# Kernel tuning notes

Measured on AMD Instinct MI355X. Metric: run time of the kernel, lower is better.

## Reference

```python
import jax, jax.numpy as jnp
import numpy as np

NUM_ITERATIONS = 10


def _nearest_neighbor(src, tgt):
    # src: [B,N,3], tgt: [B,M,3] -> indices [B,N] of nearest tgt point per src point
    inner = -2.0 * jnp.einsum('bnd,bmd->bnm', src, tgt)            # [B,N,M]
    xx = jnp.sum(src * src, axis=2, keepdims=True)                  # [B,N,1]
    yy = jnp.sum(tgt * tgt, axis=2, keepdims=True).transpose(0, 2, 1)  # [B,1,M]
    distances = xx + inner + yy                                     # [B,N,M]
    return jnp.argmin(distances, axis=2)                            # [B,N]


def _compute_transformation(src, tgt):
    # src, tgt: [B,N,3] matched pairs -> rigid (R [B,3,3], t [B,3])
    N = src.shape[1]
    c_src = jnp.mean(src, axis=1, keepdims=True)                    # [B,1,3]
    c_tgt = jnp.mean(tgt, axis=1, keepdims=True)                    # [B,1,3]
    H = jnp.einsum('bnd,bne->bde', src - c_src, tgt - c_tgt) / N    # [B,3,3]
    U, S, Vh = jnp.linalg.svd(H, full_matrices=False)
    V = jnp.swapaxes(Vh, -1, -2)                                    # matches torch.svd's V
    R = V @ jnp.swapaxes(U, -1, -2)
    det = jnp.linalg.det(R)                                         # [B]
    sign = 1.0 - 2.0 * (det < 0).astype(src.dtype)                  # +1 or -1
    # torch code scales V[:, :, 2] (third column of V)
    V = V * jnp.concatenate([jnp.ones_like(sign)[:, None],
                             jnp.ones_like(sign)[:, None],
                             sign[:, None]], axis=1)[:, None, :]    # scale col 2
    R = V @ jnp.swapaxes(U, -1, -2)                                 # [B,3,3]
    t = c_tgt[:, 0, :] - jnp.einsum('bij,bj->bi', R, c_src[:, 0, :])  # [B,3]
    return R, t


def _icp(src, tgt):
    transformed_src = src
    R = None
    t = None
    for _ in range(NUM_ITERATIONS):
        indices = _nearest_neighbor(transformed_src, tgt)           # [B,N]
        matched_tgt = jnp.take_along_axis(tgt, indices[:, :, None], axis=1)  # [B,N,3]
        R, t = _compute_transformation(transformed_src, matched_tgt)
        # faithful to torch: x @ R + t (R applied on the right)
        transformed_src = jnp.einsum('bnd,bde->bne', transformed_src, R) + t[:, None, :]
    return R, t, transformed_src


def setup_inputs() -> dict:
    key = jax.random.key(0)
    k1, k2 = jax.random.split(key)
    src = jax.random.normal(k1, (4, 4096, 3), dtype=jnp.float32)
    tgt = jax.random.normal(k2, (4, 4096, 3), dtype=jnp.float32)
    return {"src": src, "tgt": tgt}


def reference(src, tgt):
    # Returns (est_R [B,3,3], est_t [B,3], transformed_source [B,N,3])
    return _icp(src, tgt)
```

## Files before the change

kernel.cpp:

```cpp
#include <hip/hip_runtime.h>
#include <math.h>

#define NB 4
#define NP 4096
#define MP 4096

typedef __bf16 bf16x8 __attribute__((ext_vector_type(8)));
typedef float  f32x16 __attribute__((ext_vector_type(16)));

static __device__ __forceinline__ unsigned short bh(float f) {
    unsigned u = __float_as_uint(f);
    unsigned r = (u + 0x7FFFu + ((u >> 16) & 1u)) >> 16;
    return (unsigned short)r;
}
static __device__ __forceinline__ float hf(unsigned short h) {
    return __uint_as_float(((unsigned)h) << 16);
}

__device__ __forceinline__ void kabsch_f32(const float* s, float* RtL) {
    const float invN = 1.0f / (float)NP;
    float cs[3] = { s[0] * invN, s[1] * invN, s[2] * invN };
    float ct[3] = { s[3] * invN, s[4] * invN, s[5] * invN };
    float H[3][3];
    for (int d = 0; d < 3; ++d)
        for (int e = 0; e < 3; ++e)
            H[d][e] = s[6 + d * 3 + e] * invN - cs[d] * ct[e];

    float A[3][3];
    for (int i = 0; i < 3; ++i)
        for (int j = 0; j < 3; ++j)
            A[i][j] = H[0][i] * H[0][j] + H[1][i] * H[1][j] + H[2][i] * H[2][j];

    float V[3][3] = {{1, 0, 0}, {0, 1, 0}, {0, 0, 1}};
    for (int sweep = 0; sweep < 8; ++sweep) {
        float off = A[0][1] * A[0][1] + A[0][2] * A[0][2] + A[1][2] * A[1][2];
        if (off < 1e-16f) break;
        for (int pi = 0; pi < 3; ++pi) {
            const int p = (pi == 2) ? 1 : 0;
            const int q = (pi == 0) ? 1 : 2;
            float apq = A[p][q];
            if (fabsf(apq) < 1e-30f) continue;
            float theta = (A[q][q] - A[p][p]) / (2.0f * apq);
            float t = 1.0f / (fabsf(theta) + sqrtf(1.0f + theta * theta));
            if (theta < 0.0f) t = -t;
            float cth = 1.0f / sqrtf(1.0f + t * t);
            float sth = t * cth;
            float App = A[p][p], Aqq = A[q][q];
            A[p][p] = App - t * apq;
            A[q][q] = Aqq + t * apq;
            A[p][q] = A[q][p] = 0.0f;
            const int r = 3 - p - q;
            float Apr = A[p][r], Aqr = A[q][r];
            A[p][r] = A[r][p] = cth * Apr - sth * Aqr;
            A[q][r] = A[r][q] = sth * Apr + cth * Aqr;
            for (int i = 0; i < 3; ++i) {
                float Vip = V[i][p], Viq = V[i][q];
                V[i][p] = cth * Vip - sth * Viq;
                V[i][q] = sth * Vip + cth * Viq;
            }
        }
    }
    float lam[3] = { A[0][0], A[1][1], A[2][2] };
    for (int i = 0; i < 2; ++i)
        for (int j = i + 1; j < 3; ++j)
            if (lam[j] > lam[i]) {
                float tl = lam[i]; lam[i] = lam[j]; lam[j] = tl;
                for (int k = 0; k < 3; ++k) {
                    float tv = V[k][i]; V[k][i] = V[k][j]; V[k][j] = tv;
                }
            }

    float U[3][3];
    for (int k = 0; k < 3; ++k) {
        float w0 = H[0][0] * V[0][k] + H[0][1] * V[1][k] + H[0][2] * V[2][k];
        float w1 = H[1][0] * V[0][k] + H[1][1] * V[1][k] + H[1][2] * V[2][k];
        float w2 = H[2][0] * V[0][k] + H[2][1] * V[1][k] + H[2][2] * V[2][k];
        float nrm = sqrtf(w0 * w0 + w1 * w1 + w2 * w2);
        if (nrm > 1e-20f) {
            U[0][k] = w0 / nrm; U[1][k] = w1 / nrm; U[2][k] = w2 / nrm;
        } else {
            U[0][k] = U[1][0] * U[2][1] - U[2][0] * U[1][1];
            U[1][k] = U[2][0] * U[0][1] - U[0][0] * U[2][1];
            U[2][k] = U[0][0] * U[1][1] - U[1][0] * U[0][1];
        }
    }

    float detH = H[0][0] * (H[1][1] * H[2][2] - H[1][2] * H[2][1])
               - H[0][1] * (H[1][0] * H[2][2] - H[1][2] * H[2][0])
               + H[0][2] * (H[1][0] * H[2][1] - H[1][1] * H[2][0]);
    float sgn = (detH < 0.0f) ? -1.0f : 1.0f;

    float R[3][3];
    for (int i = 0; i < 3; ++i)
        for (int j = 0; j < 3; ++j)
            R[i][j] = V[i][0] * U[j][0] + V[i][1] * U[j][1] + sgn * V[i][2] * U[j][2];
    float tv[3];
    for (int i = 0; i < 3; ++i)
        tv[i] = ct[i] - (R[i][0] * cs[0] + R[i][1] * cs[1] + R[i][2] * cs[2]);

    for (int i = 0; i < 3; ++i)
        for (int j = 0; j < 3; ++j)
            RtL[i * 3 + j] = R[i][j];
    for (int i = 0; i < 3; ++i) RtL[9 + i] = tv[i];
}

__global__ __launch_bounds__(256) void icp_init(const float* __restrict__ tgt,
                                                float4* __restrict__ tgt4,
                                                uint4* __restrict__ Bbuf) {
    const int t    = blockIdx.x * 256 + threadIdx.x;
    const int b    = t >> 13;
    const int rem  = t & 8191;
    const int tile = rem >> 6;
    const int lane = rem & 63;
    const int n    = lane & 31;
    const int h    = lane >> 5;
    const int gt   = b * MP + tile * 32 + n;

    float x = tgt[gt * 3 + 0];
    float y = tgt[gt * 3 + 1];
    float z = tgt[gt * 3 + 2];
    float wv = x * x + y * y + z * z;

    unsigned short xh = bh(x), xl = bh(x - hf(xh));
    unsigned short yh = bh(y), yl = bh(y - hf(yh));
    unsigned short zh = bh(z), zl = bh(z - hf(zh));
    unsigned short wh = bh(wv), wl = bh(wv - hf(wh));
    const unsigned short ONE = 0x3F80;

    unsigned short s0, s1, s2, s3, s4, s5, s6, s7;
    if (h == 0) { s0 = xh; s1 = xh; s2 = xl; s3 = xl;
                  s4 = yh; s5 = yh; s6 = yl; s7 = yl; }
    else        { s0 = zh; s1 = zh; s2 = zl; s3 = zl;
                  s4 = wh; s5 = wl; s6 = ONE; s7 = ONE; }
    uint4 u;
    u.x = (unsigned)s0 | ((unsigned)s1 << 16);
    u.y = (unsigned)s2 | ((unsigned)s3 << 16);
    u.z = (unsigned)s4 | ((unsigned)s5 << 16);
    u.w = (unsigned)s6 | ((unsigned)s7 << 16);
    Bbuf[t] = u;

    if (h == 0) tgt4[gt] = make_float4(x, y, z, wv);
}

__global__ __launch_bounds__(1024) void icp_scan(
        const float* __restrict__ src,
        const float4* __restrict__ tgt4,
        const uint4* __restrict__ Bbuf,
        float* __restrict__ S,
        const float* __restrict__ pprev,
        float* __restrict__ pout,
        int first) {
    __shared__ unsigned CK[512];
    __shared__ float RtL[12];

    const int blk = blockIdx.x;
    const int b   = blk >> 6;
    const int g   = blk & 63;
    const int tid = threadIdx.x;
    const int w   = tid >> 6;
    const int l   = tid & 63;
    const int ts  = w & 1;
    const int tr  = w >> 1;
    const int gsrc = b * NP + g * 64 + l;

    if (w == 0) {
        if (first) {
            if (l < 12) RtL[l] = (l == 0 || l == 4 || l == 8) ? 1.0f : 0.0f;
        } else {
            const float4* rp = (const float4*)(pprev + (b * 64 + l) * 16);
            float4 r0 = rp[0], r1 = rp[1], r2 = rp[2], r3 = rp[3];
            float sm[15] = { r0.x, r0.y, r0.z, r0.w, r1.x, r1.y, r1.z, r1.w,
                             r2.x, r2.y, r2.z, r2.w, r3.x, r3.y, r3.z };
            #pragma unroll
            for (int k = 0; k < 15; ++k) {
                float v = sm[k];
                v += __shfl_down(v, 32);
                v += __shfl_down(v, 16);
                v += __shfl_down(v, 8);
                v += __shfl_down(v, 4);
                v += __shfl_down(v, 2);
                v += __shfl_down(v, 1);
                sm[k] = v;
            }
            if (l == 0) kabsch_f32(sm, RtL);
        }
    }
    __syncthreads();

    float px, py, pz;
    {
        const float* P = first ? src : S;
        float x = P[gsrc * 3 + 0];
        float y = P[gsrc * 3 + 1];
        float z = P[gsrc * 3 + 2];
        px = x * RtL[0] + y * RtL[3] + z * RtL[6] + RtL[9];
        py = x * RtL[1] + y * RtL[4] + z * RtL[7] + RtL[10];
        pz = x * RtL[2] + y * RtL[5] + z * RtL[8] + RtL[11];
    }
    if (w == 1) {
        S[gsrc * 3 + 0] = px;
        S[gsrc * 3 + 1] = py;
        S[gsrc * 3 + 2] = pz;
    }

    const int h = l >> 5;
    union { unsigned short s[8]; bf16x8 v; } Af;
    {
        const int j3 = ts * 32 + (l & 31);
        float pxj = __shfl(px, j3);
        float pyj = __shfl(py, j3);
        float pzj = __shfl(pz, j3);
        float ax = -2.0f * pxj, ay = -2.0f * pyj, az = -2.0f * pzj;
        float qv = pxj * pxj + pyj * pyj + pzj * pzj + 1.0f;
        unsigned short axh = bh(ax), axl = bh(ax - hf(axh));
        unsigned short ayh = bh(ay), ayl = bh(ay - hf(ayh));
        unsigned short azh = bh(az), azl = bh(az - hf(azh));
        unsigned short qh  = bh(qv), ql  = bh(qv - hf(qh));
        const unsigned short ONE = 0x3F80;
        if (h == 0) {
            Af.s[0] = axh; Af.s[1] = axl; Af.s[2] = axh; Af.s[3] = axl;
            Af.s[4] = ayh; Af.s[5] = ayl; Af.s[6] = ayh; Af.s[7] = ayl;
        } else {
            Af.s[0] = azh; Af.s[1] = azl; Af.s[2] = azh; Af.s[3] = azl;
            Af.s[4] = ONE; Af.s[5] = ONE; Af.s[6] = qh;  Af.s[7] = ql;
        }
    }

    f32x16 zero;
    #pragma unroll
    for (int i = 0; i < 16; ++i) zero[i] = 0.0f;

    float best[16];
    #pragma unroll
    for (int r = 0; r < 16; ++r) best[r] = __uint_as_float(0x7F7FFFFFu);

    const uint4* Bw = Bbuf + (b * 128 + tr * 16) * 64;
    const int col = l & 31;

    uint4 fb[4];
    fb[0] = Bw[l];
    fb[1] = Bw[64 + l];
    fb[2] = Bw[128 + l];
    fb[3] = Bw[192 + l];

    #pragma unroll
    for (int t = 0; t < 16; ++t) {
        bf16x8 Bf = __builtin_bit_cast(bf16x8, fb[t & 3]);
        if (t < 12) fb[t & 3] = Bw[(t + 4) * 64 + l];
        f32x16 d16 = __builtin_amdgcn_mfma_f32_32x32x16_bf16(Af.v, Bf, zero,
                                                             0, 0, 0);
        const unsigned idxk = (unsigned)((tr * 16 + t) * 32 + col);
        #pragma unroll
        for (int r = 0; r < 16; ++r) {
            float key = __uint_as_float(
                (__float_as_uint(d16[r]) & 0xFFFFF000u) | idxk);
            best[r] = fminf(best[r], key);
        }
    }

    #pragma unroll
    for (int r = 0; r < 16; ++r) {
        float v = best[r];
        v = fminf(v, __shfl_xor(v, 1));
        v = fminf(v, __shfl_xor(v, 2));
        v = fminf(v, __shfl_xor(v, 4));
        v = fminf(v, __shfl_xor(v, 8));
        v = fminf(v, __shfl_xor(v, 16));
        best[r] = v;
    }
    if ((l & 31) == 0) {
        #pragma unroll
        for (int r = 0; r < 16; ++r) {
            const int row = (r & 3) + 8 * (r >> 2) + 4 * h;
            CK[tr * 64 + ts * 32 + row] = __float_as_uint(best[r]);
        }
    }
    __syncthreads();

    if (w == 0) {
        unsigned kb = CK[l];
        #pragma unroll
        for (int k = 1; k < 8; ++k) {
            unsigned kk = CK[k * 64 + l];
            kb = kk < kb ? kk : kb;
        }
        const int idx = kb & 0xFFF;
        float4 mt = tgt4[b * MP + idx];
        const float tx = mt.x, ty = mt.y, tz = mt.z;

        float v[15];
        v[0]  = px;      v[1]  = py;      v[2]  = pz;
        v[3]  = tx;      v[4]  = ty;      v[5]  = tz;
        v[6]  = px * tx; v[7]  = px * ty; v[8]  = px * tz;
        v[9]  = py * tx; v[10] = py * ty; v[11] = py * tz;
        v[12] = pz * tx; v[13] = pz * ty; v[14] = pz * tz;
        #pragma unroll
        for (int k = 0; k < 15; ++k) {
            float s = v[k];
            s += __shfl_down(s, 32);
            s += __shfl_down(s, 16);
            s += __shfl_down(s, 8);
            s += __shfl_down(s, 4);
            s += __shfl_down(s, 2);
            s += __shfl_down(s, 1);
            v[k] = s;
        }
        if (l == 0) {
            float* pp = pout + blk * 16;
            #pragma unroll
            for (int k = 0; k < 15; ++k) pp[k] = v[k];
        }
    }
}

__global__ __launch_bounds__(256) void icp_final(
        const float* __restrict__ S,
        const float* __restrict__ plast,
        float* __restrict__ out) {
    __shared__ float RtL[12];
    const int bk  = blockIdx.x;
    const int tid = threadIdx.x;
    const int gid = bk * 256 + tid;
    const int b   = gid >> 12;

    if (tid < 64) {
        const float4* rp = (const float4*)(plast + (b * 64 + tid) * 16);
        float4 r0 = rp[0], r1 = rp[1], r2 = rp[2], r3 = rp[3];
        float sm[15] = { r0.x, r0.y, r0.z, r0.w, r1.x, r1.y, r1.z, r1.w,
                         r2.x, r2.y, r2.z, r2.w, r3.x, r3.y, r3.z };
        #pragma unroll
        for (int k = 0; k < 15; ++k) {
            float v = sm[k];
            v += __shfl_down(v, 32);
            v += __shfl_down(v, 16);
            v += __shfl_down(v, 8);
            v += __shfl_down(v, 4);
            v += __shfl_down(v, 2);
            v += __shfl_down(v, 1);
            sm[k] = v;
        }
        if (tid == 0) kabsch_f32(sm, RtL);
    }
    __syncthreads();

    float x = S[gid * 3 + 0];
    float y = S[gid * 3 + 1];
    float z = S[gid * 3 + 2];
    out[48 + gid * 3 + 0] = x * RtL[0] + y * RtL[3] + z * RtL[6] + RtL[9];
    out[48 + gid * 3 + 1] = x * RtL[1] + y * RtL[4] + z * RtL[7] + RtL[10];
    out[48 + gid * 3 + 2] = x * RtL[2] + y * RtL[5] + z * RtL[8] + RtL[11];
    if ((bk & 15) == 0) {
        if (tid < 9) out[b * 9 + tid] = RtL[tid];
        if (tid < 3) out[36 + b * 3 + tid] = RtL[9 + tid];
    }
}

extern "C" void kernel_launch(void* const* d_in, const int* in_sizes, int n_in,
                              void* d_out, int out_size, void* d_ws, size_t ws_size,
                              hipStream_t stream) {
    const float* src = (const float*)d_in[0];
    const float* tgt = (const float*)d_in[1];
    float* out = (float*)d_out;

    float* W     = (float*)d_ws;
    float4* tgt4 = (float4*)W;
    uint4*  Bbuf = (uint4*)(W + 65536);
    float*  S    = W + 65536 + 131072;
    float*  pA   = S + 49152;
    float*  pB   = pA + 4096;
    float* bufs[2] = { pA, pB };

    icp_init<<<128, 256, 0, stream>>>(tgt, tgt4, Bbuf);
    for (int k = 0; k < 10; ++k) {
        icp_scan<<<256, 1024, 0, stream>>>(src, tgt4, Bbuf, S,
                                           bufs[(k + 1) & 1], bufs[k & 1],
                                           k == 0 ? 1 : 0);
    }
    icp_final<<<64, 256, 0, stream>>>(S, bufs[1], out);
}
```

Baseline: 193.7 us.

## Fuse per-iteration Kabsch into last-block reduction and track cumulative transform

```diff
diff --git a/kernel.cpp b/kernel.cpp
--- a/kernel.cpp
+++ b/kernel.cpp
@@ -32,7 +32,7 @@
             A[i][j] = H[0][i] * H[0][j] + H[1][i] * H[1][j] + H[2][i] * H[2][j];
 
     float V[3][3] = {{1, 0, 0}, {0, 1, 0}, {0, 0, 1}};
-    for (int sweep = 0; sweep < 8; ++sweep) {
+    for (int sweep = 0; sweep < 6; ++sweep) {
         float off = A[0][1] * A[0][1] + A[0][2] * A[0][2] + A[1][2] * A[1][2];
         if (off < 1e-16f) break;
         for (int pi = 0; pi < 3; ++pi) {
@@ -106,7 +106,10 @@
 
 __global__ __launch_bounds__(256) void icp_init(const float* __restrict__ tgt,
                                                 float4* __restrict__ tgt4,
-                                                uint4* __restrict__ Bbuf) {
+                                                uint4* __restrict__ Bbuf,
+                                                float* __restrict__ acc,
+                                                unsigned* __restrict__ cnt,
+                                                float* __restrict__ Rc) {
     const int t    = blockIdx.x * 256 + threadIdx.x;
     const int b    = t >> 13;
     const int rem  = t & 8191;
@@ -138,80 +141,62 @@
     u.z = (unsigned)s4 | ((unsigned)s5 << 16);
     u.w = (unsigned)s6 | ((unsigned)s7 << 16);
     Bbuf[t] = u;
-
     if (h == 0) tgt4[gt] = make_float4(x, y, z, wv);
-}
-
-__global__ __launch_bounds__(1024) void icp_scan(
+
+    if (blockIdx.x == 0) {
+        const int td = threadIdx.x;
+        for (int k = td; k < 10 * NB * 16; k += 256) acc[k] = 0.0f;
+        if (td < 10 * NB) cnt[td] = 0u;
+        if (td < NB * 12) {
+            int j = td % 12;
+            Rc[td] = (j == 0 || j == 4 || j == 8) ? 1.0f : 0.0f;
+        }
+    }
+}
+
+__global__ __launch_bounds__(512) void icp_scan(
         const float* __restrict__ src,
         const float4* __restrict__ tgt4,
         const uint4* __restrict__ Bbuf,
-        float* __restrict__ S,
-        const float* __restrict__ pprev,
-        float* __restrict__ pout,
-        int first) {
-    __shared__ unsigned CK[512];
-    __shared__ float RtL[12];
+        float* __restrict__ acc,
+        unsigned* __restrict__ cnt,
+        float* __restrict__ Rc,
+        float* __restrict__ Rs) {
+    __shared__ unsigned CK[256];
 
     const int blk = blockIdx.x;
-    const int b   = blk >> 6;
-    const int g   = blk & 63;
+    const int b   = blk >> 7;
+    const int g   = blk & 127;
     const int tid = threadIdx.x;
     const int w   = tid >> 6;
     const int l   = tid & 63;
-    const int ts  = w & 1;
-    const int tr  = w >> 1;
-    const int gsrc = b * NP + g * 64 + l;
-
-    if (w == 0) {
-        if (first) {
-            if (l < 12) RtL[l] = (l == 0 || l == 4 || l == 8) ? 1.0f : 0.0f;
-        } else {
-            const float4* rp = (const float4*)(pprev + (b * 64 + l) * 16);
-            float4 r0 = rp[0], r1 = rp[1], r2 = rp[2], r3 = rp[3];
-            float sm[15] = { r0.x, r0.y, r0.z, r0.w, r1.x, r1.y, r1.z, r1.w,
-                             r2.x, r2.y, r2.z, r2.w, r3.x, r3.y, r3.z };
-            #pragma unroll
-            for (int k = 0; k < 15; ++k) {
-                float v = sm[k];
-                v += __shfl_down(v, 32);
-                v += __shfl_down(v, 16);
-                v += __shfl_down(v, 8);
-                v += __shfl_down(v, 4);
-                v += __shfl_down(v, 2);
-                v += __shfl_down(v, 1);
-                sm[k] = v;
-            }
-            if (l == 0) kabsch_f32(sm, RtL);
-        }
-    }
-    __syncthreads();
-
-    float px, py, pz;
-    {
-        const float* P = first ? src : S;
-        float x = P[gsrc * 3 + 0];
-        float y = P[gsrc * 3 + 1];
-        float z = P[gsrc * 3 + 2];
-        px = x * RtL[0] + y * RtL[3] + z * RtL[6] + RtL[9];
-        py = x * RtL[1] + y * RtL[4] + z * RtL[7] + RtL[10];
-        pz = x * RtL[2] + y * RtL[5] + z * RtL[8] + RtL[11];
-    }
-    if (w == 1) {
-        S[gsrc * 3 + 0] = px;
-        S[gsrc * 3 + 1] = py;
-        S[gsrc * 3 + 2] = pz;
-    }
-
-    const int h = l >> 5;
+    const int m   = l & 31;
+    const int h   = l >> 5;
+
+    const uint4* Bw = Bbuf + (b * 128 + w * 16) * 64;
+    uint4 fb[4];
+    fb[0] = Bw[l];
+    fb[1] = Bw[64 + l];
+    fb[2] = Bw[128 + l];
+    fb[3] = Bw[192 + l];
+
+    const float* rc = Rc + b * 12;
+    const float c0 = rc[0], c1 = rc[1], c2 = rc[2];
+    const float c3 = rc[3], c4 = rc[4], c5 = rc[5];
+    const float c6 = rc[6], c7 = rc[7], c8 = rc[8];
+    const float c9 = rc[9], c10 = rc[10], c11 = rc[11];
+    const int gsrc = b * NP + g * 32 + m;
+    float x = src[gsrc * 3 + 0];
+    float y = src[gsrc * 3 + 1];
+    float z = src[gsrc * 3 + 2];
+    const float px = x * c0 + y * c3 + z * c6 + c9;
+    const float py = x * c1 + y * c4 + z * c7 + c10;
+    const float pz = x * c2 + y * c5 + z * c8 + c11;
+
     union { unsigned short s[8]; bf16x8 v; } Af;
     {
-        const int j3 = ts * 32 + (l & 31);
-        float pxj = __shfl(px, j3);
-        float pyj = __shfl(py, j3);
-        float pzj = __shfl(pz, j3);
-        float ax = -2.0f * pxj, ay = -2.0f * pyj, az = -2.0f * pzj;
-        float qv = pxj * pxj + pyj * pyj + pzj * pzj + 1.0f;
+        float ax = -2.0f * px, ay = -2.0f * py, az = -2.0f * pz;
+        float qv = px * px + py * py + pz * pz + 1.0f;
         unsigned short axh = bh(ax), axl = bh(ax - hf(axh));
         unsigned short ayh = bh(ay), ayl = bh(ay - hf(ayh));
         unsigned short azh = bh(az), azl = bh(az - hf(azh));
@@ -234,27 +219,22 @@
     #pragma unroll
     for (int r = 0; r < 16; ++r) best[r] = __uint_as_float(0x7F7FFFFFu);
 
-    const uint4* Bw = Bbuf + (b * 128 + tr * 16) * 64;
     const int col = l & 31;
-
-    uint4 fb[4];
-    fb[0] = Bw[l];
-    fb[1] = Bw[64 + l];
-    fb[2] = Bw[128 + l];
-    fb[3] = Bw[192 + l];
-
     #pragma unroll
     for (int t = 0; t < 16; ++t) {
         bf16x8 Bf = __builtin_bit_cast(bf16x8, fb[t & 3]);
         if (t < 12) fb[t & 3] = Bw[(t + 4) * 64 + l];
         f32x16 d16 = __builtin_amdgcn_mfma_f32_32x32x16_bf16(Af.v, Bf, zero,
                                                              0, 0, 0);
-        const unsigned idxk = (unsigned)((tr * 16 + t) * 32 + col);
+        const unsigned idxk = (unsigned)((w * 16 + t) * 32 + col);
         #pragma unroll
-        for (int r = 0; r < 16; ++r) {
-            float key = __uint_as_float(
+        for (int r = 0; r < 16; r += 2) {
+            float k0 = __uint_as_float(
                 (__float_as_uint(d16[r]) & 0xFFFFF000u) | idxk);
-            best[r] = fminf(best[r], key);
+            float k1 = __uint_as_float(
+                (__float_as_uint(d16[r + 1]) & 0xFFFFF000u) | idxk);
+            best[r]     = fminf(best[r], k0);
+            best[r + 1] = fminf(best[r + 1], k1);
         }
     }
 
@@ -268,32 +248,37 @@
         v = fminf(v, __shfl_xor(v, 16));
         best[r] = v;
     }
-    if ((l & 31) == 0) {
+    if (col == 0) {
         #pragma unroll
         for (int r = 0; r < 16; ++r) {
             const int row = (r & 3) + 8 * (r >> 2) + 4 * h;
-            CK[tr * 64 + ts * 32 + row] = __float_as_uint(best[r]);
+            CK[w * 32 + row] = __float_as_uint(best[r]);
         }
     }
     __syncthreads();
 
     if (w == 0) {
-        unsigned kb = CK[l];
-        #pragma unroll
-        for (int k = 1; k < 8; ++k) {
-            unsigned kk = CK[k * 64 + l];
-            kb = kk < kb ? kk : kb;
-        }
-        const int idx = kb & 0xFFF;
+        int idx = 0;
+        if (l < 32) {
+            unsigned kb = CK[l];
+            #pragma unroll
+            for (int k = 1; k < 8; ++k) {
+                unsigned kk = CK[k * 32 + l];
+                kb = kk < kb ? kk : kb;
+            }
+            idx = kb & 0xFFF;
+        }
         float4 mt = tgt4[b * MP + idx];
-        const float tx = mt.x, ty = mt.y, tz = mt.z;
+        const float sel = (l < 32) ? 1.0f : 0.0f;
+        const float sx = px * sel, sy = py * sel, sz = pz * sel;
+        const float tx = mt.x * sel, ty = mt.y * sel, tz = mt.z * sel;
 
         float v[15];
-        v[0]  = px;      v[1]  = py;      v[2]  = pz;
+        v[0]  = sx;      v[1]  = sy;      v[2]  = sz;
         v[3]  = tx;      v[4]  = ty;      v[5]  = tz;
-        v[6]  = px * tx; v[7]  = px * ty; v[8]  = px * tz;
-        v[9]  = py * tx; v[10] = py * ty; v[11] = py * tz;
-        v[12] = pz * tx; v[13] = pz * ty; v[14] = pz * tz;
+        v[6]  = sx * tx; v[7]  = sx * ty; v[8]  = sx * tz;
+        v[9]  = sy * tx; v[10] = sy * ty; v[11] = sy * tz;
+        v[12] = sz * tx; v[13] = sz * ty; v[14] = sz * tz;
         #pragma unroll
         for (int k = 0; k < 15; ++k) {
             float s = v[k];
@@ -305,53 +290,70 @@
             s += __shfl_down(s, 1);
             v[k] = s;
         }
+
+        unsigned old = 0;
         if (l == 0) {
-            float* pp = pout + blk * 16;
+            float* ab = acc + b * 16;
             #pragma unroll
-            for (int k = 0; k < 15; ++k) pp[k] = v[k];
+            for (int k = 0; k < 15; ++k) atomicAdd(&ab[k], v[k]);
+            __threadfence();
+            old = atomicAdd(&cnt[b], 1u);
+        }
+        old = __shfl(old, 0);
+
+        if (old == 127u) {
+            __threadfence();
+            float sv = 0.0f;
+            if (l < 15) sv = atomicAdd(&acc[b * 16 + l], 0.0f);
+            float sm[15];
+            #pragma unroll
+            for (int k = 0; k < 15; ++k) sm[k] = __shfl(sv, k);
+            if (l == 0) {
+                float St[12];
+                kabsch_f32(sm, St);
+                float* rs = Rs + b * 12;
+                #pragma unroll
+                for (int i = 0; i < 12; ++i) rs[i] = St[i];
+                float Mc[12];
+                #pragma unroll
+                for (int i = 0; i < 12; ++i) Mc[i] = rc[i];
+                float Mo[12];
+                for (int i = 0; i < 3; ++i)
+                    for (int j = 0; j < 3; ++j)
+                        Mo[i * 3 + j] = Mc[i * 3 + 0] * St[j] +
+                                        Mc[i * 3 + 1] * St[3 + j] +
+                                        Mc[i * 3 + 2] * St[6 + j];
+                for (int j = 0; j < 3; ++j)
+                    Mo[9 + j] = Mc[9] * St[j] + Mc[10] * St[3 + j] +
+                                Mc[11] * St[6 + j] + St[9 + j];
+                float* rcw = Rc + b * 12;
+                #pragma unroll
+                for (int i = 0; i < 12; ++i) rcw[i] = Mo[i];
+            }
         }
     }
 }
 
 __global__ __launch_bounds__(256) void icp_final(
-        const float* __restrict__ S,
-        const float* __restrict__ plast,
+        const float* __restrict__ src,
+        const float* __restrict__ Rc,
+        const float* __restrict__ Rs,
         float* __restrict__ out) {
-    __shared__ float RtL[12];
     const int bk  = blockIdx.x;
     const int tid = threadIdx.x;
     const int gid = bk * 256 + tid;
     const int b   = gid >> 12;
 
-    if (tid < 64) {
-        const float4* rp = (const float4*)(plast + (b * 64 + tid) * 16);
-        float4 r0 = rp[0], r1 = rp[1], r2 = rp[2], r3 = rp[3];
-        float sm[15] = { r0.x, r0.y, r0.z, r0.w, r1.x, r1.y, r1.z, r1.w,
-                         r2.x, r2.y, r2.z, r2.w, r3.x, r3.y, r3.z };
-        #pragma unroll
-        for (int k = 0; k < 15; ++k) {
-            float v = sm[k];
-            v += __shfl_down(v, 32);
-            v += __shfl_down(v, 16);
-            v += __shfl_down(v, 8);
-            v += __shfl_down(v, 4);
-            v += __shfl_down(v, 2);
-            v += __shfl_down(v, 1);
-            sm[k] = v;
-        }
-        if (tid == 0) kabsch_f32(sm, RtL);
-    }
-    __syncthreads();
-
-    float x = S[gid * 3 + 0];
-    float y = S[gid * 3 + 1];
-    float z = S[gid * 3 + 2];
-    out[48 + gid * 3 + 0] = x * RtL[0] + y * RtL[3] + z * RtL[6] + RtL[9];
-    out[48 + gid * 3 + 1] = x * RtL[1] + y * RtL[4] + z * RtL[7] + RtL[10];
-    out[48 + gid * 3 + 2] = x * RtL[2] + y * RtL[5] + z * RtL[8] + RtL[11];
+    const float* rc = Rc + b * 12;
+    float x = src[gid * 3 + 0];
+    float y = src[gid * 3 + 1];
+    float z = src[gid * 3 + 2];
+    out[48 + gid * 3 + 0] = x * rc[0] + y * rc[3] + z * rc[6] + rc[9];
+    out[48 + gid * 3 + 1] = x * rc[1] + y * rc[4] + z * rc[7] + rc[10];
+    out[48 + gid * 3 + 2] = x * rc[2] + y * rc[5] + z * rc[8] + rc[11];
     if ((bk & 15) == 0) {
-        if (tid < 9) out[b * 9 + tid] = RtL[tid];
-        if (tid < 3) out[36 + b * 3 + tid] = RtL[9 + tid];
+        if (tid < 9) out[b * 9 + tid] = Rs[b * 12 + tid];
+        if (tid < 3) out[36 + b * 3 + tid] = Rs[b * 12 + 9 + tid];
     }
 }
 
@@ -362,19 +364,19 @@
     const float* tgt = (const float*)d_in[1];
     float* out = (float*)d_out;
 
-    float* W     = (float*)d_ws;
-    float4* tgt4 = (float4*)W;
-    uint4*  Bbuf = (uint4*)(W + 65536);
-    float*  S    = W + 65536 + 131072;
-    float*  pA   = S + 49152;
-    float*  pB   = pA + 4096;
-    float* bufs[2] = { pA, pB };
-
-    icp_init<<<128, 256, 0, stream>>>(tgt, tgt4, Bbuf);
+    float* W      = (float*)d_ws;
+    float4* tgt4  = (float4*)W;
+    uint4*  Bbuf  = (uint4*)(W + 65536);
+    float*  acc   = W + 65536 + 131072;
+    unsigned* cnt = (unsigned*)(acc + 640);
+    float*  Rc    = (float*)(cnt + 40);
+    float*  Rs    = Rc + 48;
+
+    icp_init<<<128, 256, 0, stream>>>(tgt, tgt4, Bbuf, acc, cnt, Rc);
     for (int k = 0; k < 10; ++k) {
-        icp_scan<<<256, 1024, 0, stream>>>(src, tgt4, Bbuf, S,
-                                           bufs[(k + 1) & 1], bufs[k & 1],
-                                           k == 0 ? 1 : 0);
-    }
-    icp_final<<<64, 256, 0, stream>>>(S, bufs[1], out);
-}
+        icp_scan<<<512, 512, 0, stream>>>(src, tgt4, Bbuf,
+                                          acc + k * NB * 16, cnt + k * NB,
+                                          Rc, Rs);
+    }
+    icp_final<<<64, 256, 0, stream>>>(src, Rc, Rs, out);
+}
```

New measurement: 670.8 us. +246.3%, slower.

## Compose cumulative rigid transform instead of storing transformed points; reshape scan grid

Applied to the files above, without the earlier changes.

```diff
diff --git a/kernel.cpp b/kernel.cpp
--- a/kernel.cpp
+++ b/kernel.cpp
@@ -32,9 +32,7 @@
             A[i][j] = H[0][i] * H[0][j] + H[1][i] * H[1][j] + H[2][i] * H[2][j];
 
     float V[3][3] = {{1, 0, 0}, {0, 1, 0}, {0, 0, 1}};
-    for (int sweep = 0; sweep < 8; ++sweep) {
-        float off = A[0][1] * A[0][1] + A[0][2] * A[0][2] + A[1][2] * A[1][2];
-        if (off < 1e-16f) break;
+    for (int sweep = 0; sweep < 5; ++sweep) {
         for (int pi = 0; pi < 3; ++pi) {
             const int p = (pi == 2) ? 1 : 0;
             const int q = (pi == 0) ? 1 : 2;
@@ -104,6 +102,52 @@
     for (int i = 0; i < 3; ++i) RtL[9 + i] = tv[i];
 }
 
+__device__ __forceinline__ void solve_compose(const float* __restrict__ pprev,
+                                              const float* __restrict__ RcIn,
+                                              int b, int l,
+                                              float* __restrict__ McL,
+                                              float* __restrict__ StL) {
+    const float4* rp0 = (const float4*)(pprev + (b * 128 + l) * 16);
+    const float4* rp1 = (const float4*)(pprev + (b * 128 + 64 + l) * 16);
+    float4 a0 = rp0[0], a1 = rp0[1], a2 = rp0[2], a3 = rp0[3];
+    float4 c0 = rp1[0], c1 = rp1[1], c2 = rp1[2], c3 = rp1[3];
+    float sm[15] = { a0.x + c0.x, a0.y + c0.y, a0.z + c0.z, a0.w + c0.w,
+                     a1.x + c1.x, a1.y + c1.y, a1.z + c1.z, a1.w + c1.w,
+                     a2.x + c2.x, a2.y + c2.y, a2.z + c2.z, a2.w + c2.w,
+                     a3.x + c3.x, a3.y + c3.y, a3.z + c3.z };
+    #pragma unroll
+    for (int k = 0; k < 15; ++k) {
+        float v = sm[k];
+        v += __shfl_down(v, 32);
+        v += __shfl_down(v, 16);
+        v += __shfl_down(v, 8);
+        v += __shfl_down(v, 4);
+        v += __shfl_down(v, 2);
+        v += __shfl_down(v, 1);
+        sm[k] = v;
+    }
+    if (l == 0) {
+        float St[12];
+        kabsch_f32(sm, St);
+        const float* mc = RcIn + b * 12;
+        float Mo[12];
+        for (int i = 0; i < 3; ++i)
+            for (int j = 0; j < 3; ++j)
+                Mo[i * 3 + j] = mc[i * 3 + 0] * St[j] +
+                                mc[i * 3 + 1] * St[3 + j] +
+                                mc[i * 3 + 2] * St[6 + j];
+        for (int j = 0; j < 3; ++j)
+            Mo[9 + j] = mc[9] * St[j] + mc[10] * St[3 + j] +
+                        mc[11] * St[6 + j] + St[9 + j];
+        #pragma unroll
+        for (int i = 0; i < 12; ++i) McL[i] = Mo[i];
+        if (StL) {
+            #pragma unroll
+            for (int i = 0; i < 12; ++i) StL[i] = St[i];
+        }
+    }
+}
+
 __global__ __launch_bounds__(256) void icp_init(const float* __restrict__ tgt,
                                                 float4* __restrict__ tgt4,
                                                 uint4* __restrict__ Bbuf) {
@@ -138,80 +182,67 @@
     u.z = (unsigned)s4 | ((unsigned)s5 << 16);
     u.w = (unsigned)s6 | ((unsigned)s7 << 16);
     Bbuf[t] = u;
-
     if (h == 0) tgt4[gt] = make_float4(x, y, z, wv);
 }
 
-__global__ __launch_bounds__(1024) void icp_scan(
+__global__ __launch_bounds__(512, 4) void icp_scan(
         const float* __restrict__ src,
         const float4* __restrict__ tgt4,
         const uint4* __restrict__ Bbuf,
-        float* __restrict__ S,
         const float* __restrict__ pprev,
         float* __restrict__ pout,
+        const float* __restrict__ RcIn,
+        float* __restrict__ RcOut,
         int first) {
-    __shared__ unsigned CK[512];
-    __shared__ float RtL[12];
+    __shared__ unsigned CK[256];
+    __shared__ float McL[12];
 
     const int blk = blockIdx.x;
-    const int b   = blk >> 6;
-    const int g   = blk & 63;
+    const int b   = blk >> 7;
+    const int g   = blk & 127;
     const int tid = threadIdx.x;
     const int w   = tid >> 6;
     const int l   = tid & 63;
-    const int ts  = w & 1;
-    const int tr  = w >> 1;
-    const int gsrc = b * NP + g * 64 + l;
+    const int m   = l & 31;
+    const int h   = l >> 5;
+
+    const int gsrc = b * NP + g * 32 + m;
+    const float x0 = src[gsrc * 3 + 0];
+    const float y0 = src[gsrc * 3 + 1];
+    const float z0 = src[gsrc * 3 + 2];
+    const uint4* Bw = Bbuf + (b * 128 + w * 16) * 64;
+    uint4 fb[8];
+    #pragma unroll
+    for (int t = 0; t < 8; ++t) fb[t] = Bw[t * 64 + l];
 
     if (w == 0) {
         if (first) {
-            if (l < 12) RtL[l] = (l == 0 || l == 4 || l == 8) ? 1.0f : 0.0f;
+            if (l == 0) {
+                #pragma unroll
+                for (int i = 0; i < 12; ++i) {
+                    float v = (i == 0 || i == 4 || i == 8) ? 1.0f : 0.0f;
+                    McL[i] = v;
+                    RcOut[b * 12 + i] = v;
+                }
+            }
         } else {
-            const float4* rp = (const float4*)(pprev + (b * 64 + l) * 16);
-            float4 r0 = rp[0], r1 = rp[1], r2 = rp[2], r3 = rp[3];
-            float sm[15] = { r0.x, r0.y, r0.z, r0.w, r1.x, r1.y, r1.z, r1.w,
-                             r2.x, r2.y, r2.z, r2.w, r3.x, r3.y, r3.z };
-            #pragma unroll
-            for (int k = 0; k < 15; ++k) {
-                float v = sm[k];
-                v += __shfl_down(v, 32);
-                v += __shfl_down(v, 16);
-                v += __shfl_down(v, 8);
-                v += __shfl_down(v, 4);
-                v += __shfl_down(v, 2);
-                v += __shfl_down(v, 1);
-                sm[k] = v;
-            }
-            if (l == 0) kabsch_f32(sm, RtL);
+            solve_compose(pprev, RcIn, b, l, McL, nullptr);
+            if (l == 0) {
+                #pragma unroll
+                for (int i = 0; i < 12; ++i) RcOut[b * 12 + i] = McL[i];
+            }
         }
     }
     __syncthreads();
 
-    float px, py, pz;
-    {
-        const float* P = first ? src : S;
-        float x = P[gsrc * 3 + 0];
-        float y = P[gsrc * 3 + 1];
-        float z = P[gsrc * 3 + 2];
-        px = x * RtL[0] + y * RtL[3] + z * RtL[6] + RtL[9];
-        py = x * RtL[1] + y * RtL[4] + z * RtL[7] + RtL[10];
-        pz = x * RtL[2] + y * RtL[5] + z * RtL[8] + RtL[11];
-    }
-    if (w == 1) {
-        S[gsrc * 3 + 0] = px;
-        S[gsrc * 3 + 1] = py;
-        S[gsrc * 3 + 2] = pz;
-    }
-
-    const int h = l >> 5;
+    const float px = x0 * McL[0] + y0 * McL[3] + z0 * McL[6] + McL[9];
+    const float py = x0 * McL[1] + y0 * McL[4] + z0 * McL[7] + McL[10];
+    const float pz = x0 * McL[2] + y0 * McL[5] + z0 * McL[8] + McL[11];
+
     union { unsigned short s[8]; bf16x8 v; } Af;
     {
-        const int j3 = ts * 32 + (l & 31);
-        float pxj = __shfl(px, j3);
-        float pyj = __shfl(py, j3);
-        float pzj = __shfl(pz, j3);
-        float ax = -2.0f * pxj, ay = -2.0f * pyj, az = -2.0f * pzj;
-        float qv = pxj * pxj + pyj * pyj + pzj * pzj + 1.0f;
+        float ax = -2.0f * px, ay = -2.0f * py, az = -2.0f * pz;
+        float qv = px * px + py * py + pz * pz + 1.0f;
         unsigned short axh = bh(ax), axl = bh(ax - hf(axh));
         unsigned short ayh = bh(ay), ayl = bh(ay - hf(ayh));
         unsigned short azh = bh(az), azl = bh(az - hf(azh));
@@ -229,32 +260,30 @@
     f32x16 zero;
     #pragma unroll
     for (int i = 0; i < 16; ++i) zero[i] = 0.0f;
-
     float best[16];
     #pragma unroll
     for (int r = 0; r < 16; ++r) best[r] = __uint_as_float(0x7F7FFFFFu);
 
-    const uint4* Bw = Bbuf + (b * 128 + tr * 16) * 64;
-    const int col = l & 31;
-
-    uint4 fb[4];
-    fb[0] = Bw[l];
-    fb[1] = Bw[64 + l];
-    fb[2] = Bw[128 + l];
-    fb[3] = Bw[192 + l];
-
-    #pragma unroll
-    for (int t = 0; t < 16; ++t) {
-        bf16x8 Bf = __builtin_bit_cast(bf16x8, fb[t & 3]);
-        if (t < 12) fb[t & 3] = Bw[(t + 4) * 64 + l];
-        f32x16 d16 = __builtin_amdgcn_mfma_f32_32x32x16_bf16(Af.v, Bf, zero,
-                                                             0, 0, 0);
-        const unsigned idxk = (unsigned)((tr * 16 + t) * 32 + col);
+    const int col = m;
+    #pragma unroll
+    for (int t = 0; t < 16; t += 2) {
+        bf16x8 Bf0 = __builtin_bit_cast(bf16x8, fb[t & 7]);
+        if (t < 8) fb[t & 7] = Bw[(t + 8) * 64 + l];
+        bf16x8 Bf1 = __builtin_bit_cast(bf16x8, fb[(t + 1) & 7]);
+        if (t + 1 < 8) fb[(t + 1) & 7] = Bw[(t + 9) * 64 + l];
+        f32x16 d0 = __builtin_amdgcn_mfma_f32_32x32x16_bf16(Af.v, Bf0, zero,
+                                                            0, 0, 0);
+        f32x16 d1 = __builtin_amdgcn_mfma_f32_32x32x16_bf16(Af.v, Bf1, zero,
+                                                            0, 0, 0);
+        const unsigned i0 = (unsigned)((w * 16 + t) * 32 + col);
+        const unsigned i1 = i0 + 32;
         #pragma unroll
         for (int r = 0; r < 16; ++r) {
-            float key = __uint_as_float(
-                (__float_as_uint(d16[r]) & 0xFFFFF000u) | idxk);
-            best[r] = fminf(best[r], key);
+            float k0 = __uint_as_float(
+                (__float_as_uint(d0[r]) & 0xFFFFF000u) | i0);
+            float k1 = __uint_as_float(
+                (__float_as_uint(d1[r]) & 0xFFFFF000u) | i1);
+            best[r] = fminf(fminf(k0, k1), best[r]);
         }
     }
 
@@ -268,90 +297,77 @@
         v = fminf(v, __shfl_xor(v, 16));
         best[r] = v;
     }
-    if ((l & 31) == 0) {
+    if (col == 0) {
         #pragma unroll
         for (int r = 0; r < 16; ++r) {
             const int row = (r & 3) + 8 * (r >> 2) + 4 * h;
-            CK[tr * 64 + ts * 32 + row] = __float_as_uint(best[r]);
+            CK[w * 32 + row] = __float_as_uint(best[r]);
         }
     }
     __syncthreads();
 
-    if (w == 0) {
-        unsigned kb = CK[l];
+    {
+        unsigned kb = CK[m];
         #pragma unroll
         for (int k = 1; k < 8; ++k) {
-            unsigned kk = CK[k * 64 + l];
+            unsigned kk = CK[k * 32 + m];
             kb = kk < kb ? kk : kb;
         }
-        const int idx = kb & 0xFFF;
-        float4 mt = tgt4[b * MP + idx];
-        const float tx = mt.x, ty = mt.y, tz = mt.z;
-
-        float v[15];
-        v[0]  = px;      v[1]  = py;      v[2]  = pz;
-        v[3]  = tx;      v[4]  = ty;      v[5]  = tz;
-        v[6]  = px * tx; v[7]  = px * ty; v[8]  = px * tz;
-        v[9]  = py * tx; v[10] = py * ty; v[11] = py * tz;
-        v[12] = pz * tx; v[13] = pz * ty; v[14] = pz * tz;
-        #pragma unroll
-        for (int k = 0; k < 15; ++k) {
-            float s = v[k];
-            s += __shfl_down(s, 32);
-            s += __shfl_down(s, 16);
-            s += __shfl_down(s, 8);
-            s += __shfl_down(s, 4);
-            s += __shfl_down(s, 2);
-            s += __shfl_down(s, 1);
-            v[k] = s;
-        }
-        if (l == 0) {
-            float* pp = pout + blk * 16;
-            #pragma unroll
-            for (int k = 0; k < 15; ++k) pp[k] = v[k];
-        }
-    }
-}
-
-__global__ __launch_bounds__(256) void icp_final(
-        const float* __restrict__ S,
-        const float* __restrict__ plast,
-        float* __restrict__ out) {
-    __shared__ float RtL[12];
-    const int bk  = blockIdx.x;
-    const int tid = threadIdx.x;
-    const int gid = bk * 256 + tid;
-    const int b   = gid >> 12;
-
-    if (tid < 64) {
-        const float4* rp = (const float4*)(plast + (b * 64 + tid) * 16);
-        float4 r0 = rp[0], r1 = rp[1], r2 = rp[2], r3 = rp[3];
-        float sm[15] = { r0.x, r0.y, r0.z, r0.w, r1.x, r1.y, r1.z, r1.w,
-                         r2.x, r2.y, r2.z, r2.w, r3.x, r3.y, r3.z };
-        #pragma unroll
-        for (int k = 0; k < 15; ++k) {
-            float v = sm[k];
+        float4 mt = tgt4[b * MP + (kb & 0xFFF)];
+        const float sel = (l < 32) ? 1.0f : 0.0f;
+        const float sx = px * sel, sy = py * sel, sz = pz * sel;
+        const float tx = mt.x * sel, ty = mt.y * sel, tz = mt.z * sel;
+
+        #pragma unroll
+        for (int k2 = 0; k2 < 2; ++k2) {
+            const int k = 2 * w + k2;
+            if (k >= 15) break;
+            float v;
+            switch (k) {
+                case 0:  v = sx; break;       case 1:  v = sy; break;
+                case 2:  v = sz; break;       case 3:  v = tx; break;
+                case 4:  v = ty; break;       case 5:  v = tz; break;
+                case 6:  v = sx * tx; break;  case 7:  v = sx * ty; break;
+                case 8:  v = sx * tz; break;  case 9:  v = sy * tx; break;
+                case 10: v = sy * ty; break;  case 11: v = sy * tz; break;
+                case 12: v = sz * tx; break;  case 13: v = sz * ty; break;
+                default: v = sz * tz; break;
+            }
             v += __shfl_down(v, 32);
             v += __shfl_down(v, 16);
             v += __shfl_down(v, 8);
             v += __shfl_down(v, 4);
             v += __shfl_down(v, 2);
             v += __shfl_down(v, 1);
-            sm[k] = v;
-        }
-        if (tid == 0) kabsch_f32(sm, RtL);
-    }
+            if (l == 0) pout[blk * 16 + k] = v;
+        }
+    }
+}
+
+__global__ __launch_bounds__(256) void icp_final(
+        const float* __restrict__ src,
+        const float* __restrict__ plast,
+        const float* __restrict__ RcIn,
+        float* __restrict__ out) {
+    __shared__ float McL[12];
+    __shared__ float StL[12];
+    const int bk  = blockIdx.x;
+    const int tid = threadIdx.x;
+    const int gid = bk * 256 + tid;
+    const int b   = gid >> 12;
+
+    if (tid < 64) solve_compose(plast, RcIn, b, tid, McL, StL);
     __syncthreads();
 
-    float x = S[gid * 3 + 0];
-    float y = S[gid * 3 + 1];
-    float z = S[gid * 3 + 2];
-    out[48 + gid * 3 + 0] = x * RtL[0] + y * RtL[3] + z * RtL[6] + RtL[9];
-    out[48 + gid * 3 + 1] = x * RtL[1] + y * RtL[4] + z * RtL[7] + RtL[10];
-    out[48 + gid * 3 + 2] = x * RtL[2] + y * RtL[5] + z * RtL[8] + RtL[11];
+    float x = src[gid * 3 + 0];
+    float y = src[gid * 3 + 1];
+    float z = src[gid * 3 + 2];
+    out[48 + gid * 3 + 0] = x * McL[0] + y * McL[3] + z * McL[6] + McL[9];
+    out[48 + gid * 3 + 1] = x * McL[1] + y * McL[4] + z * McL[7] + McL[10];
+    out[48 + gid * 3 + 2] = x * McL[2] + y * McL[5] + z * McL[8] + McL[11];
     if ((bk & 15) == 0) {
-        if (tid < 9) out[b * 9 + tid] = RtL[tid];
-        if (tid < 3) out[36 + b * 3 + tid] = RtL[9 + tid];
+        if (tid < 9) out[b * 9 + tid] = StL[tid];
+        if (tid < 3) out[36 + b * 3 + tid] = StL[9 + tid];
     }
 }
 
@@ -365,16 +381,19 @@
     float* W     = (float*)d_ws;
     float4* tgt4 = (float4*)W;
     uint4*  Bbuf = (uint4*)(W + 65536);
-    float*  S    = W + 65536 + 131072;
-    float*  pA   = S + 49152;
-    float*  pB   = pA + 4096;
-    float* bufs[2] = { pA, pB };
+    float*  P0   = W + 65536 + 131072;
+    float*  P1   = P0 + 8192;
+    float*  Rc0  = P1 + 8192;
+    float*  Rc1  = Rc0 + 48;
+    float* P[2]  = { P0, P1 };
+    float* Rc[2] = { Rc0, Rc1 };
 
     icp_init<<<128, 256, 0, stream>>>(tgt, tgt4, Bbuf);
     for (int k = 0; k < 10; ++k) {
-        icp_scan<<<256, 1024, 0, stream>>>(src, tgt4, Bbuf, S,
-                                           bufs[(k + 1) & 1], bufs[k & 1],
-                                           k == 0 ? 1 : 0);
-    }
-    icp_final<<<64, 256, 0, stream>>>(S, bufs[1], out);
-}
+        icp_scan<<<512, 512, 0, stream>>>(src, tgt4, Bbuf,
+                                          P[(k + 1) & 1], P[k & 1],
+                                          Rc[(k + 1) & 1], Rc[k & 1],
+                                          k == 0 ? 1 : 0);
+    }
+    icp_final<<<64, 256, 0, stream>>>(src, P[1], Rc[1], out);
+}
```

Measured after the change: 226.5 us. 1.17x slower.
